# Kernel optimization log

Hardware: AMD Instinct MI355X
Metric: run time of the kernel (lower is better)

## Reference

```python
import jax, jax.numpy as jnp
import numpy as np

BATCH = 128
VOCAB = 128000


def setup_inputs() -> dict:
    key = jax.random.key(0)
    k1, k2, k3, k4 = jax.random.split(key, 4)
    logits = jax.random.normal(k1, (BATCH, VOCAB), dtype=jnp.float32)
    # per-row top-k in [1, VOCAB] (k == VOCAB means "no top-k filtering")
    k = jax.random.randint(k2, (BATCH,), 1, VOCAB + 1, dtype=jnp.int64)
    # per-row top-p in (0, 1)
    p = jax.random.uniform(k3, (BATCH,), dtype=jnp.float32, minval=0.05, maxval=0.99)
    # exponential noise for Gumbel-like weighted sampling (vLLM random_sample)
    exp_noise = jax.random.exponential(k4, (BATCH, VOCAB), dtype=jnp.float32)
    return {"logits": logits, "k": k, "p": p, "exp_noise": exp_noise}


def _apply_top_k_top_p(logits, k, p):
    vocab = logits.shape[1]
    probs = jax.nn.softmax(logits, axis=-1)           # [B, V]
    probs_sort = jnp.sort(probs, axis=-1)             # ascending, [B, V]

    # --- top-k: find cutoff = k-th largest prob (ties included) ---
    top_k_count = (vocab - k.astype(jnp.int32))[:, None]          # [B, 1]
    top_k_cutoff = jnp.take_along_axis(probs_sort, top_k_count, axis=-1)  # [B, 1]
    no_top_k_mask = (k.astype(jnp.int32) == vocab)[:, None]
    top_k_cutoff = jnp.where(no_top_k_mask, -jnp.inf, top_k_cutoff)
    logits = jnp.where(probs < top_k_cutoff, -jnp.inf, logits)

    # --- top-p: cutoff = smallest prob kept so that kept mass >= p ---
    cumprob = jnp.cumsum(probs_sort, axis=-1)                      # [B, V]
    top_p_mask = cumprob <= (1.0 - p[:, None])
    top_p_mask = top_p_mask.at[:, -1].set(False)  # keep at least one token
    top_p_count = jnp.sum(top_p_mask, axis=-1, keepdims=True)      # [B, 1]
    top_p_cutoff = jnp.take_along_axis(probs_sort, top_p_count, axis=-1)
    logits = jnp.where(probs < top_p_cutoff, -jnp.inf, logits)
    return logits


def reference(logits, k, p, exp_noise):
    filtered = _apply_top_k_top_p(logits, k, p)
    probs = jax.nn.softmax(filtered.astype(jnp.float32), axis=-1)  # [B, V]
    # vLLM random_sample: probs / Exp(1) noise, argmax == categorical draw
    samples = jnp.argmax(probs / exp_noise, axis=-1)               # [B]
    return samples
```

## Files before the change

### kernel.cpp

```cpp
#include <hip/hip_runtime.h>
#include <math.h>
#include <limits.h>

#define V 128000
#define R 128
#define NB 4096
#define NT 1024
#define SLICES 4
#define SLICE (V / SLICES)
#define S4 (SLICE / 4)
#define CAP 1024
#define BPT (NB / NT)

typedef unsigned long long u64;

struct Rec {
    u64   Tu;
    u64   psPu;
    float rowmax;
    float Lcut;
    int   binK;
    int   rankK;
    int   binP;
    int   binP2;
    unsigned pcP;
    unsigned minP2;
    int   nK;
    int   nP;
};

__device__ __forceinline__ int binof(float x) {
    int b = (int)floorf((x + 8.0f) * 256.0f);
    b = b < 0 ? 0 : b;
    b = b > NB - 1 ? NB - 1 : b;
    return b;
}

__device__ __forceinline__ u64 expq(float x) {
    float xc = fminf(x, 14.0f);
    return (u64)(expf(xc) * 16777216.0f);
}

__device__ __forceinline__ unsigned fmono(float x) {
    unsigned b = __float_as_uint(x);
    return b ^ ((b >> 31) ? 0xFFFFFFFFu : 0x80000000u);
}
__device__ __forceinline__ float fmono_inv(unsigned m) {
    unsigned b = (m & 0x80000000u) ? (m ^ 0x80000000u) : ~m;
    return __uint_as_float(b);
}

__device__ __forceinline__ bool better(float v1, int i1, float v2, int i2) {
    bool n1 = (v1 != v1), n2 = (v2 != v2);
    if (n1 != n2) return n1;
    if (n1) return i1 < i2;
    if (v1 != v2) return v1 > v2;
    return i1 < i2;
}

__global__ __launch_bounds__(NT) void k1_hist(
    const float* __restrict__ logits,
    unsigned* __restrict__ histCnt, u64* __restrict__ histSum,
    float* __restrict__ sliceMax)
{
    const int row = blockIdx.x / SLICES;
    const int sl  = blockIdx.x % SLICES;
    const int tid = threadIdx.x;
    const float4* l4 = reinterpret_cast<const float4*>(logits + (size_t)row * V) + (size_t)sl * S4;

    __shared__ unsigned hc[NB];
    __shared__ u64      hs[NB];
    __shared__ float    redf[NT];

    for (int i = tid; i < NB; i += NT) { hc[i] = 0u; hs[i] = 0ull; }
    __syncthreads();

    float lmax = -INFINITY;
    for (int i = tid; i < S4; i += NT) {
        float4 q = l4[i];
        float xs[4] = {q.x, q.y, q.z, q.w};
        #pragma unroll
        for (int c = 0; c < 4; ++c) {
            float x = xs[c];
            lmax = fmaxf(lmax, x);
            int b = binof(x);
            atomicAdd(&hc[b], 1u);
            atomicAdd(&hs[b], expq(x));
        }
    }
    redf[tid] = lmax;
    __syncthreads();
    for (int s = NT / 2; s > 0; s >>= 1) {
        if (tid < s) redf[tid] = fmaxf(redf[tid], redf[tid + s]);
        __syncthreads();
    }

    unsigned* gc = histCnt + ((size_t)sl * R + row) * NB;
    u64*      gs = histSum + ((size_t)sl * R + row) * NB;
    for (int i = tid; i < NB; i += NT) { gc[i] = hc[i]; gs[i] = hs[i]; }
    if (tid == 0) sliceMax[row * SLICES + sl] = redf[0];
}

__global__ __launch_bounds__(NT) void k2a_scan(
    const unsigned* __restrict__ histCnt, const u64* __restrict__ histSum,
    const float* __restrict__ sliceMax,
    const int* __restrict__ kk, const float* __restrict__ pp,
    Rec* __restrict__ rec)
{
    const int row = blockIdx.x;
    const int tid = threadIdx.x;

    __shared__ unsigned hcnt[NB];
    __shared__ u64      hsum[NB];
    __shared__ unsigned chCnt[NT];
    __shared__ u64      chSum[NT];
    __shared__ u64 s_psPu;
    __shared__ int s_binK, s_rankK, s_binP, s_binP2;
    __shared__ unsigned s_pcP;

    if (tid == 0) {
        s_binK = -1; s_rankK = 0; s_binP = -1; s_binP2 = NB;
        s_pcP = 0u; s_psPu = 0ull;
    }

    for (int i = tid; i < NB; i += NT) {
        unsigned c = 0; u64 s = 0ull;
        #pragma unroll
        for (int sl = 0; sl < SLICES; ++sl) {
            c += histCnt[((size_t)sl * R + row) * NB + i];
            s += histSum[((size_t)sl * R + row) * NB + i];
        }
        hcnt[i] = c; hsum[i] = s;
    }
    __syncthreads();

    const int kv = kk[row];
    const float pv = pp[row];

    unsigned cc = 0; u64 cs = 0ull;
    #pragma unroll
    for (int j = 0; j < BPT; ++j) { cc += hcnt[tid * BPT + j]; cs += hsum[tid * BPT + j]; }
    chCnt[tid] = cc; chSum[tid] = cs;
    __syncthreads();
    for (int off = 1; off < NT; off <<= 1) {
        unsigned uc = chCnt[tid]; u64 uf = chSum[tid];
        unsigned ac = (tid >= off) ? chCnt[tid - off] : 0u;
        u64      af = (tid >= off) ? chSum[tid - off] : 0ull;
        __syncthreads();
        chCnt[tid] = uc + ac; chSum[tid] = uf + af;
        __syncthreads();
    }
    const u64 Zu = chSum[NT - 1];
    const float omp = 1.0f - pv;
    const u64 Tu = (u64)((double)omp * (double)Zu);

    {
        unsigned pc = (tid > 0) ? chCnt[tid - 1] : 0u;
        u64 ps = (tid > 0) ? chSum[tid - 1] : 0ull;
        const unsigned rk = (unsigned)(V - kv);
        #pragma unroll
        for (int j = 0; j < BPT; ++j) {
            int bin = tid * BPT + j;
            unsigned c = hcnt[bin]; u64 s = hsum[bin];
            if (kv < V && c > 0u && rk >= pc && rk < pc + c) {
                s_binK = bin; s_rankK = (int)(rk - pc);
            }
            if (c > 0u && ps <= Tu && ps + s > Tu) {
                if (atomicCAS(&s_binP, -1, bin) == -1) { s_pcP = pc; s_psPu = ps; }
            }
            pc += c; ps += s;
        }
    }
    __syncthreads();
    if (tid == 0 && s_binP < 0) {
        unsigned pc = 0u; u64 ps = 0ull;
        int lastb = -1; unsigned lastpc = 0u; u64 lastps = 0ull;
        for (int b = 0; b < NB; ++b) {
            unsigned c = hcnt[b]; u64 s = hsum[b];
            if (c > 0u) {
                if (ps <= Tu && ps + s > Tu) { s_binP = b; s_pcP = pc; s_psPu = ps; break; }
                lastb = b; lastpc = pc; lastps = ps;
            }
            pc += c; ps += s;
        }
        if (s_binP < 0) { s_binP = lastb; s_pcP = lastpc; s_psPu = lastps; }
    }
    __syncthreads();
    {
        const int bp = s_binP;
        #pragma unroll
        for (int j = 0; j < BPT; ++j) {
            int bin = tid * BPT + j;
            if (bin > bp && hcnt[bin] > 0u) atomicMin(&s_binP2, bin);
        }
    }
    __syncthreads();

    if (tid == 0) {
        float rm = sliceMax[row * SLICES + 0];
        #pragma unroll
        for (int sl = 1; sl < SLICES; ++sl) rm = fmaxf(rm, sliceMax[row * SLICES + sl]);
        Rec rc;
        rc.Tu = Tu; rc.psPu = s_psPu;
        rc.rowmax = rm; rc.Lcut = -INFINITY;
        rc.binK = s_binK; rc.rankK = s_rankK; rc.binP = s_binP; rc.binP2 = s_binP2;
        rc.pcP = s_pcP; rc.minP2 = 0xFFFFFFFFu; rc.nK = 0; rc.nP = 0;
        rec[row] = rc;
    }
}

__global__ __launch_bounds__(NT) void k2b_collect(
    const float* __restrict__ logits, Rec* __restrict__ rec,
    float* __restrict__ candK, float* __restrict__ candP)
{
    const int row = blockIdx.x / SLICES;
    const int sl  = blockIdx.x % SLICES;
    const int tid = threadIdx.x;
    const float4* l4 = reinterpret_cast<const float4*>(logits + (size_t)row * V) + (size_t)sl * S4;

    const int bK = rec[row].binK, bP = rec[row].binP, bP2 = rec[row].binP2;
    float* cK = candK + (size_t)row * CAP;
    float* cP = candP + (size_t)row * CAP;

    for (int i = tid; i < S4; i += NT) {
        float4 q = l4[i];
        float xs[4] = {q.x, q.y, q.z, q.w};
        #pragma unroll
        for (int c = 0; c < 4; ++c) {
            float x = xs[c];
            int b = binof(x);
            if (b == bK) { int pos = atomicAdd(&rec[row].nK, 1); if (pos < CAP) cK[pos] = x; }
            if (b == bP) { int pos = atomicAdd(&rec[row].nP, 1); if (pos < CAP) cP[pos] = x; }
            if (b == bP2) atomicMin(&rec[row].minP2, fmono(x));
        }
    }
}

__global__ __launch_bounds__(NT) void k2c_cutoff(
    const int* __restrict__ kk, Rec* __restrict__ rec,
    const float* __restrict__ candK, const float* __restrict__ candP)
{
    const int row = blockIdx.x;
    const int tid = threadIdx.x;

    __shared__ float lcK[CAP];
    __shared__ float lcP[CAP];
    __shared__ float sorted[CAP];
    __shared__ float s_cutK;

    if (tid == 0) s_cutK = -INFINITY;
    const int kv = kk[row];
    const Rec rc = rec[row];
    const int nK = min(rc.nK, CAP), nP = min(rc.nP, CAP);

    if (tid < nK) lcK[tid] = candK[(size_t)row * CAP + tid];
    if (tid < nP) lcP[tid] = candP[(size_t)row * CAP + tid];
    __syncthreads();

    if (kv < V && tid < nK) {
        float v = lcK[tid];
        int r = 0;
        for (int j = 0; j < nK; ++j) {
            float u = lcK[j];
            r += (int)((u < v) | ((u == v) & (j < tid)));
        }
        if (r == rc.rankK) s_cutK = v;
    }
    if (tid < nP) {
        float v = lcP[tid];
        int r = 0;
        for (int j = 0; j < nP; ++j) {
            float u = lcP[j];
            r += (int)((u < v) | ((u == v) & (j < tid)));
        }
        sorted[r] = v;
    }
    __syncthreads();

    if (tid == 0) {
        float cutP;
        if (nP <= 0) {
            cutP = -INFINITY;
        } else {
            u64 cum = rc.psPu; int cin = 0;
            while (cin < nP) {
                u64 nc = cum + expq(sorted[cin]);
                if (nc <= rc.Tu) { cum = nc; ++cin; } else break;
            }
            long cglob = (long)rc.pcP + cin;
            if (cglob > (long)(V - 1)) cglob = V - 1;
            int local = (int)(cglob - (long)rc.pcP);
            cutP = (local < nP) ? sorted[local] : fmono_inv(rc.minP2);
        }
        float cutK = (kv < V) ? s_cutK : -INFINITY;
        rec[row].Lcut = fmaxf(cutK, cutP);
    }
}

__global__ __launch_bounds__(NT) void k3_argmax(
    const float* __restrict__ logits, const float* __restrict__ noise,
    const Rec* __restrict__ rec, float* __restrict__ partV, int* __restrict__ partI)
{
    const int row = blockIdx.x / SLICES;
    const int sl  = blockIdx.x % SLICES;
    const int tid = threadIdx.x;
    const float4* l4 = reinterpret_cast<const float4*>(logits + (size_t)row * V) + (size_t)sl * S4;
    const float4* n4 = reinterpret_cast<const float4*>(noise  + (size_t)row * V) + (size_t)sl * S4;
    const int base = sl * SLICE;

    __shared__ float redf[NT];
    __shared__ int   redi[NT];

    const float Lcut = rec[row].Lcut, rmax = rec[row].rowmax;
    float bv = -INFINITY; int bi = INT_MAX;
    for (int i = tid; i < S4; i += NT) {
        float4 lq = l4[i];
        float4 nq = n4[i];
        float ls[4] = {lq.x, lq.y, lq.z, lq.w};
        float ns[4] = {nq.x, nq.y, nq.z, nq.w};
        #pragma unroll
        for (int c = 0; c < 4; ++c) {
            int idx = base + 4 * i + c;
            float prob = (ls[c] >= Lcut) ? expf(ls[c] - rmax) : 0.0f;
            float r = prob / ns[c];
            if (better(r, idx, bv, bi)) { bv = r; bi = idx; }
        }
    }
    redf[tid] = bv; redi[tid] = bi;
    __syncthreads();
    for (int s = NT / 2; s > 0; s >>= 1) {
        if (tid < s) {
            if (better(redf[tid + s], redi[tid + s], redf[tid], redi[tid])) {
                redf[tid] = redf[tid + s]; redi[tid] = redi[tid + s];
            }
        }
        __syncthreads();
    }
    if (tid == 0) { partV[row * SLICES + sl] = redf[0]; partI[row * SLICES + sl] = redi[0]; }
}

__global__ __launch_bounds__(R) void k4_final(
    const float* __restrict__ partV, const int* __restrict__ partI, int* __restrict__ out)
{
    const int row = threadIdx.x;
    float bv = partV[row * SLICES + 0]; int bi = partI[row * SLICES + 0];
    #pragma unroll
    for (int sl = 1; sl < SLICES; ++sl) {
        float v = partV[row * SLICES + sl]; int i = partI[row * SLICES + sl];
        if (better(v, i, bv, bi)) { bv = v; bi = i; }
    }
    out[row] = bi;
}

__global__ __launch_bounds__(NT) void topk_topp_sample_mono(
    const float* __restrict__ logits, const int* __restrict__ kk,
    const float* __restrict__ pp, const float* __restrict__ noise,
    int* __restrict__ out)
{
    const int row = blockIdx.x;
    const int tid = threadIdx.x;
    const float4* l4 = reinterpret_cast<const float4*>(logits + (size_t)row * V);
    const float4* n4 = reinterpret_cast<const float4*>(noise  + (size_t)row * V);

    __shared__ unsigned hcnt[NB];
    __shared__ u64      hsum[NB];
    __shared__ unsigned chCnt[NT];
    __shared__ u64      chSum[NT];
    __shared__ float    redf[NT];
    __shared__ int      redi[NT];
    __shared__ float    candK[CAP];
    __shared__ float    candP[CAP];
    __shared__ float s_rowmax, s_cutK, s_Lcut;
    __shared__ u64 s_psPu;
    __shared__ int s_binK, s_rankK, s_binP, s_binP2, s_nK, s_nP;
    __shared__ unsigned s_pcP, s_minP2;

    const int kv = kk[row];
    const float pv = pp[row];

    for (int i = tid; i < NB; i += NT) { hcnt[i] = 0u; hsum[i] = 0ull; }
    if (tid == 0) {
        s_binK = -1; s_rankK = 0; s_binP = -1; s_binP2 = NB;
        s_nK = 0; s_nP = 0; s_minP2 = 0xFFFFFFFFu; s_cutK = -INFINITY;
        s_pcP = 0u; s_psPu = 0ull;
    }
    __syncthreads();

    float lmax = -INFINITY;
    for (int i = tid; i < V / 4; i += NT) {
        float4 q = l4[i];
        float xs[4] = {q.x, q.y, q.z, q.w};
        #pragma unroll
        for (int c = 0; c < 4; ++c) {
            float x = xs[c];
            lmax = fmaxf(lmax, x);
            int b = binof(x);
            atomicAdd(&hcnt[b], 1u);
            atomicAdd(&hsum[b], expq(x));
        }
    }
    redf[tid] = lmax;
    __syncthreads();
    for (int s = NT / 2; s > 0; s >>= 1) {
        if (tid < s) redf[tid] = fmaxf(redf[tid], redf[tid + s]);
        __syncthreads();
    }
    if (tid == 0) s_rowmax = redf[0];

    unsigned cc = 0; u64 cs = 0ull;
    #pragma unroll
    for (int j = 0; j < BPT; ++j) { cc += hcnt[tid * BPT + j]; cs += hsum[tid * BPT + j]; }
    chCnt[tid] = cc; chSum[tid] = cs;
    __syncthreads();
    for (int off = 1; off < NT; off <<= 1) {
        unsigned uc = chCnt[tid]; u64 uf = chSum[tid];
        unsigned ac = (tid >= off) ? chCnt[tid - off] : 0u;
        u64      af = (tid >= off) ? chSum[tid - off] : 0ull;
        __syncthreads();
        chCnt[tid] = uc + ac; chSum[tid] = uf + af;
        __syncthreads();
    }
    const u64 Zu = chSum[NT - 1];
    const float omp = 1.0f - pv;
    const u64 Tu = (u64)((double)omp * (double)Zu);

    {
        unsigned pc = (tid > 0) ? chCnt[tid - 1] : 0u;
        u64 ps = (tid > 0) ? chSum[tid - 1] : 0ull;
        const unsigned rk = (unsigned)(V - kv);
        #pragma unroll
        for (int j = 0; j < BPT; ++j) {
            int bin = tid * BPT + j;
            unsigned c = hcnt[bin]; u64 s = hsum[bin];
            if (kv < V && c > 0u && rk >= pc && rk < pc + c) {
                s_binK = bin; s_rankK = (int)(rk - pc);
            }
            if (c > 0u && ps <= Tu && ps + s > Tu) {
                if (atomicCAS(&s_binP, -1, bin) == -1) { s_pcP = pc; s_psPu = ps; }
            }
            pc += c; ps += s;
        }
    }
    __syncthreads();
    if (tid == 0 && s_binP < 0) {
        unsigned pc = 0u; u64 ps = 0ull;
        int lastb = -1; unsigned lastpc = 0u; u64 lastps = 0ull;
        for (int b = 0; b < NB; ++b) {
            unsigned c = hcnt[b]; u64 s = hsum[b];
            if (c > 0u) {
                if (ps <= Tu && ps + s > Tu) { s_binP = b; s_pcP = pc; s_psPu = ps; break; }
                lastb = b; lastpc = pc; lastps = ps;
            }
            pc += c; ps += s;
        }
        if (s_binP < 0) { s_binP = lastb; s_pcP = lastpc; s_psPu = lastps; }
    }
    __syncthreads();
    {
        const int bp = s_binP;
        #pragma unroll
        for (int j = 0; j < BPT; ++j) {
            int bin = tid * BPT + j;
            if (bin > bp && hcnt[bin] > 0u) atomicMin(&s_binP2, bin);
        }
    }
    __syncthreads();

    {
        const int bK = s_binK, bP = s_binP, bP2 = s_binP2;
        for (int i = tid; i < V / 4; i += NT) {
            float4 q = l4[i];
            float xs[4] = {q.x, q.y, q.z, q.w};
            #pragma unroll
            for (int c = 0; c < 4; ++c) {
                float x = xs[c];
                int b = binof(x);
                if (b == bK) { int pos = atomicAdd(&s_nK, 1); if (pos < CAP) candK[pos] = x; }
                if (b == bP) { int pos = atomicAdd(&s_nP, 1); if (pos < CAP) candP[pos] = x; }
                if (b == bP2) atomicMin(&s_minP2, fmono(x));
            }
        }
    }
    __syncthreads();

    const int nK = min(s_nK, CAP), nP = min(s_nP, CAP);
    if (kv < V && tid < nK) {
        float v = candK[tid];
        int r = 0;
        for (int j = 0; j < nK; ++j) {
            float u = candK[j];
            r += (int)((u < v) | ((u == v) & (j < tid)));
        }
        if (r == s_rankK) s_cutK = v;
    }
    if (tid < nP) {
        float v = candP[tid];
        int r = 0;
        for (int j = 0; j < nP; ++j) {
            float u = candP[j];
            r += (int)((u < v) | ((u == v) & (j < tid)));
        }
        redf[r] = v;
    }
    __syncthreads();
    if (tid == 0) {
        float cutP;
        if (nP <= 0) {
            cutP = -INFINITY;
        } else {
            u64 cum = s_psPu; int cin = 0;
            while (cin < nP) {
                u64 nc = cum + expq(redf[cin]);
                if (nc <= Tu) { cum = nc; ++cin; } else break;
            }
            long cglob = (long)s_pcP + cin;
            if (cglob > (long)(V - 1)) cglob = V - 1;
            int local = (int)(cglob - (long)s_pcP);
            cutP = (local < nP) ? redf[local] : fmono_inv(s_minP2);
        }
        float cutK = (kv < V) ? s_cutK : -INFINITY;
        s_Lcut = fmaxf(cutK, cutP);
    }
    __syncthreads();

    const float Lcut = s_Lcut, rmax = s_rowmax;
    float bv = -INFINITY; int bi = INT_MAX;
    for (int i = tid; i < V / 4; i += NT) {
        float4 lq = l4[i];
        float4 nq = n4[i];
        float ls[4] = {lq.x, lq.y, lq.z, lq.w};
        float ns[4] = {nq.x, nq.y, nq.z, nq.w};
        #pragma unroll
        for (int c = 0; c < 4; ++c) {
            int idx = 4 * i + c;
            float prob = (ls[c] >= Lcut) ? expf(ls[c] - rmax) : 0.0f;
            float r = prob / ns[c];
            if (better(r, idx, bv, bi)) { bv = r; bi = idx; }
        }
    }
    redf[tid] = bv; redi[tid] = bi;
    __syncthreads();
    for (int s = NT / 2; s > 0; s >>= 1) {
        if (tid < s) {
            if (better(redf[tid + s], redi[tid + s], redf[tid], redi[tid])) {
                redf[tid] = redf[tid + s]; redi[tid] = redi[tid + s];
            }
        }
        __syncthreads();
    }
    if (tid == 0) out[row] = redi[0];
}

static inline size_t alignup(size_t x) { return (x + 255) & ~(size_t)255; }

extern "C" void kernel_launch(void* const* d_in, const int* in_sizes, int n_in,
                              void* d_out, int out_size, void* d_ws, size_t ws_size,
                              hipStream_t stream) {
    const float* logits = (const float*)d_in[0];
    const int*   kk     = (const int*)d_in[1];
    const float* pp     = (const float*)d_in[2];
    const float* noise  = (const float*)d_in[3];
    int* out = (int*)d_out;
    char* ws = (char*)d_ws;

    size_t o = 0;
    size_t histCntOff = o; o = alignup(o + (size_t)SLICES * R * NB * 4);
    size_t histSumOff = o; o = alignup(o + (size_t)SLICES * R * NB * 8);
    size_t sliceMaxOff = o; o = alignup(o + (size_t)R * SLICES * 4);
    size_t recOff = o; o = alignup(o + (size_t)R * sizeof(Rec));
    size_t candKOff = o; o = alignup(o + (size_t)R * CAP * 4);
    size_t candPOff = o; o = alignup(o + (size_t)R * CAP * 4);
    size_t partVOff = o; o = alignup(o + (size_t)R * SLICES * 4);
    size_t partIOff = o; o = alignup(o + (size_t)R * SLICES * 4);

    if (ws_size >= o) {
        unsigned* histCnt = (unsigned*)(ws + histCntOff);
        u64*      histSum = (u64*)(ws + histSumOff);
        float*    sliceMax = (float*)(ws + sliceMaxOff);
        Rec*      rec = (Rec*)(ws + recOff);
        float*    candK = (float*)(ws + candKOff);
        float*    candP = (float*)(ws + candPOff);
        float*    partV = (float*)(ws + partVOff);
        int*      partI = (int*)(ws + partIOff);
        k1_hist<<<R * SLICES, NT, 0, stream>>>(logits, histCnt, histSum, sliceMax);
        k2a_scan<<<R, NT, 0, stream>>>(histCnt, histSum, sliceMax, kk, pp, rec);
        k2b_collect<<<R * SLICES, NT, 0, stream>>>(logits, rec, candK, candP);
        k2c_cutoff<<<R, NT, 0, stream>>>(kk, rec, candK, candP);
        k3_argmax<<<R * SLICES, NT, 0, stream>>>(logits, noise, rec, partV, partI);
        k4_final<<<1, R, 0, stream>>>(partV, partI, out);
        return;
    }
    topk_topp_sample_mono<<<R, NT, 0, stream>>>(logits, kk, pp, noise, out);
}
```

Baseline: 112.6 us.

## Fuse scan, collect and cutoff kernels; fold final argmax into last-arriving block

Merges the histogram scan, candidate collection and cutoff computation into one per-row kernel that keeps candidates and counters in shared memory instead of global atomics and workspace. The final per-row reduction kernel is removed: the last slice block of each row, detected via an atomic counter, combines the partial argmaxes. This cuts two kernel launches and the global round trips for the row record and candidate buffers. In exchange, collection now scans each row's logits with only 128 blocks instead of 512, which lowers parallelism on that pass.

```diff
diff --git a/kernel.cpp b/kernel.cpp
--- a/kernel.cpp
+++ b/kernel.cpp
@@ -14,19 +14,9 @@
 
 typedef unsigned long long u64;
 
-struct Rec {
-    u64   Tu;
-    u64   psPu;
+struct Cut {
+    float Lcut;
     float rowmax;
-    float Lcut;
-    int   binK;
-    int   rankK;
-    int   binP;
-    int   binP2;
-    unsigned pcP;
-    unsigned minP2;
-    int   nK;
-    int   nP;
 };
 
 __device__ __forceinline__ int binof(float x) {
@@ -101,11 +91,11 @@
     if (tid == 0) sliceMax[row * SLICES + sl] = redf[0];
 }
 
-__global__ __launch_bounds__(NT) void k2a_scan(
+__global__ __launch_bounds__(NT) void k2_cutoff(
     const unsigned* __restrict__ histCnt, const u64* __restrict__ histSum,
-    const float* __restrict__ sliceMax,
-    const int* __restrict__ kk, const float* __restrict__ pp,
-    Rec* __restrict__ rec)
+    const float* __restrict__ sliceMax, const int* __restrict__ kk,
+    const float* __restrict__ pp, const float* __restrict__ logits,
+    Cut* __restrict__ cut, unsigned* __restrict__ counters)
 {
     const int row = blockIdx.x;
     const int tid = threadIdx.x;
@@ -114,13 +104,18 @@
     __shared__ u64      hsum[NB];
     __shared__ unsigned chCnt[NT];
     __shared__ u64      chSum[NT];
+    __shared__ float    candK[CAP];
+    __shared__ float    candP[CAP];
+    __shared__ float    sorted[CAP];
     __shared__ u64 s_psPu;
-    __shared__ int s_binK, s_rankK, s_binP, s_binP2;
-    __shared__ unsigned s_pcP;
+    __shared__ float s_cutK;
+    __shared__ int s_binK, s_rankK, s_binP, s_binP2, s_nK, s_nP;
+    __shared__ unsigned s_pcP, s_minP2;
 
     if (tid == 0) {
         s_binK = -1; s_rankK = 0; s_binP = -1; s_binP2 = NB;
         s_pcP = 0u; s_psPu = 0ull;
+        s_nK = 0; s_nP = 0; s_minP2 = 0xFFFFFFFFu; s_cutK = -INFINITY;
     }
 
     for (int i = tid; i < NB; i += NT) {
@@ -196,81 +191,39 @@
     }
     __syncthreads();
 
-    if (tid == 0) {
-        float rm = sliceMax[row * SLICES + 0];
-        #pragma unroll
-        for (int sl = 1; sl < SLICES; ++sl) rm = fmaxf(rm, sliceMax[row * SLICES + sl]);
-        Rec rc;
-        rc.Tu = Tu; rc.psPu = s_psPu;
-        rc.rowmax = rm; rc.Lcut = -INFINITY;
-        rc.binK = s_binK; rc.rankK = s_rankK; rc.binP = s_binP; rc.binP2 = s_binP2;
-        rc.pcP = s_pcP; rc.minP2 = 0xFFFFFFFFu; rc.nK = 0; rc.nP = 0;
-        rec[row] = rc;
-    }
-}
-
-__global__ __launch_bounds__(NT) void k2b_collect(
-    const float* __restrict__ logits, Rec* __restrict__ rec,
-    float* __restrict__ candK, float* __restrict__ candP)
-{
-    const int row = blockIdx.x / SLICES;
-    const int sl  = blockIdx.x % SLICES;
-    const int tid = threadIdx.x;
-    const float4* l4 = reinterpret_cast<const float4*>(logits + (size_t)row * V) + (size_t)sl * S4;
-
-    const int bK = rec[row].binK, bP = rec[row].binP, bP2 = rec[row].binP2;
-    float* cK = candK + (size_t)row * CAP;
-    float* cP = candP + (size_t)row * CAP;
-
-    for (int i = tid; i < S4; i += NT) {
-        float4 q = l4[i];
-        float xs[4] = {q.x, q.y, q.z, q.w};
-        #pragma unroll
-        for (int c = 0; c < 4; ++c) {
-            float x = xs[c];
-            int b = binof(x);
-            if (b == bK) { int pos = atomicAdd(&rec[row].nK, 1); if (pos < CAP) cK[pos] = x; }
-            if (b == bP) { int pos = atomicAdd(&rec[row].nP, 1); if (pos < CAP) cP[pos] = x; }
-            if (b == bP2) atomicMin(&rec[row].minP2, fmono(x));
-        }
-    }
-}
-
-__global__ __launch_bounds__(NT) void k2c_cutoff(
-    const int* __restrict__ kk, Rec* __restrict__ rec,
-    const float* __restrict__ candK, const float* __restrict__ candP)
-{
-    const int row = blockIdx.x;
-    const int tid = threadIdx.x;
-
-    __shared__ float lcK[CAP];
-    __shared__ float lcP[CAP];
-    __shared__ float sorted[CAP];
-    __shared__ float s_cutK;
-
-    if (tid == 0) s_cutK = -INFINITY;
-    const int kv = kk[row];
-    const Rec rc = rec[row];
-    const int nK = min(rc.nK, CAP), nP = min(rc.nP, CAP);
-
-    if (tid < nK) lcK[tid] = candK[(size_t)row * CAP + tid];
-    if (tid < nP) lcP[tid] = candP[(size_t)row * CAP + tid];
-    __syncthreads();
-
+    {
+        const int bK = s_binK, bP = s_binP, bP2 = s_binP2;
+        const float4* l4 = reinterpret_cast<const float4*>(logits + (size_t)row * V);
+        for (int i = tid; i < V / 4; i += NT) {
+            float4 q = l4[i];
+            float xs[4] = {q.x, q.y, q.z, q.w};
+            #pragma unroll
+            for (int c = 0; c < 4; ++c) {
+                float x = xs[c];
+                int b = binof(x);
+                if (b == bK) { int pos = atomicAdd(&s_nK, 1); if (pos < CAP) candK[pos] = x; }
+                if (b == bP) { int pos = atomicAdd(&s_nP, 1); if (pos < CAP) candP[pos] = x; }
+                if (b == bP2) atomicMin(&s_minP2, fmono(x));
+            }
+        }
+    }
+    __syncthreads();
+
+    const int nK = min(s_nK, CAP), nP = min(s_nP, CAP);
     if (kv < V && tid < nK) {
-        float v = lcK[tid];
+        float v = candK[tid];
         int r = 0;
         for (int j = 0; j < nK; ++j) {
-            float u = lcK[j];
+            float u = candK[j];
             r += (int)((u < v) | ((u == v) & (j < tid)));
         }
-        if (r == rc.rankK) s_cutK = v;
+        if (r == s_rankK) s_cutK = v;
     }
     if (tid < nP) {
-        float v = lcP[tid];
+        float v = candP[tid];
         int r = 0;
         for (int j = 0; j < nP; ++j) {
-            float u = lcP[j];
+            float u = candP[j];
             r += (int)((u < v) | ((u == v) & (j < tid)));
         }
         sorted[r] = v;
@@ -282,24 +235,30 @@
         if (nP <= 0) {
             cutP = -INFINITY;
         } else {
-            u64 cum = rc.psPu; int cin = 0;
+            u64 cum = s_psPu; int cin = 0;
             while (cin < nP) {
                 u64 nc = cum + expq(sorted[cin]);
-                if (nc <= rc.Tu) { cum = nc; ++cin; } else break;
-            }
-            long cglob = (long)rc.pcP + cin;
+                if (nc <= Tu) { cum = nc; ++cin; } else break;
+            }
+            long cglob = (long)s_pcP + cin;
             if (cglob > (long)(V - 1)) cglob = V - 1;
-            int local = (int)(cglob - (long)rc.pcP);
-            cutP = (local < nP) ? sorted[local] : fmono_inv(rc.minP2);
+            int local = (int)(cglob - (long)s_pcP);
+            cutP = (local < nP) ? sorted[local] : fmono_inv(s_minP2);
         }
         float cutK = (kv < V) ? s_cutK : -INFINITY;
-        rec[row].Lcut = fmaxf(cutK, cutP);
+        float rm = sliceMax[row * SLICES + 0];
+        #pragma unroll
+        for (int sl = 1; sl < SLICES; ++sl) rm = fmaxf(rm, sliceMax[row * SLICES + sl]);
+        Cut c; c.Lcut = fmaxf(cutK, cutP); c.rowmax = rm;
+        cut[row] = c;
+        counters[row] = 0u;
     }
 }
 
 __global__ __launch_bounds__(NT) void k3_argmax(
     const float* __restrict__ logits, const float* __restrict__ noise,
-    const Rec* __restrict__ rec, float* __restrict__ partV, int* __restrict__ partI)
+    const Cut* __restrict__ cut, float* __restrict__ partV, int* __restrict__ partI,
+    unsigned* __restrict__ counters, int* __restrict__ out)
 {
     const int row = blockIdx.x / SLICES;
     const int sl  = blockIdx.x % SLICES;
@@ -311,7 +270,7 @@
     __shared__ float redf[NT];
     __shared__ int   redi[NT];
 
-    const float Lcut = rec[row].Lcut, rmax = rec[row].rowmax;
+    const float Lcut = cut[row].Lcut, rmax = cut[row].rowmax;
     float bv = -INFINITY; int bi = INT_MAX;
     for (int i = tid; i < S4; i += NT) {
         float4 lq = l4[i];
@@ -336,20 +295,24 @@
         }
         __syncthreads();
     }
-    if (tid == 0) { partV[row * SLICES + sl] = redf[0]; partI[row * SLICES + sl] = redi[0]; }
-}
-
-__global__ __launch_bounds__(R) void k4_final(
-    const float* __restrict__ partV, const int* __restrict__ partI, int* __restrict__ out)
-{
-    const int row = threadIdx.x;
-    float bv = partV[row * SLICES + 0]; int bi = partI[row * SLICES + 0];
-    #pragma unroll
-    for (int sl = 1; sl < SLICES; ++sl) {
-        float v = partV[row * SLICES + sl]; int i = partI[row * SLICES + sl];
-        if (better(v, i, bv, bi)) { bv = v; bi = i; }
-    }
-    out[row] = bi;
+    if (tid == 0) {
+        partV[row * SLICES + sl] = redf[0];
+        partI[row * SLICES + sl] = redi[0];
+        __threadfence();
+        unsigned old = atomicAdd(&counters[row], 1u);
+        if (old == SLICES - 1) {
+            __threadfence();
+            volatile const float* pv = partV + row * SLICES;
+            volatile const int*   pi = partI + row * SLICES;
+            float fv = pv[0]; int fi = pi[0];
+            #pragma unroll
+            for (int s2 = 1; s2 < SLICES; ++s2) {
+                float v = pv[s2]; int i2 = pi[s2];
+                if (better(v, i2, fv, fi)) { fv = v; fi = i2; }
+            }
+            out[row] = fi;
+        }
+    }
 }
 
 __global__ __launch_bounds__(NT) void topk_topp_sample_mono(
@@ -567,27 +530,22 @@
     size_t histCntOff = o; o = alignup(o + (size_t)SLICES * R * NB * 4);
     size_t histSumOff = o; o = alignup(o + (size_t)SLICES * R * NB * 8);
     size_t sliceMaxOff = o; o = alignup(o + (size_t)R * SLICES * 4);
-    size_t recOff = o; o = alignup(o + (size_t)R * sizeof(Rec));
-    size_t candKOff = o; o = alignup(o + (size_t)R * CAP * 4);
-    size_t candPOff = o; o = alignup(o + (size_t)R * CAP * 4);
+    size_t cutOff = o; o = alignup(o + (size_t)R * sizeof(Cut));
     size_t partVOff = o; o = alignup(o + (size_t)R * SLICES * 4);
     size_t partIOff = o; o = alignup(o + (size_t)R * SLICES * 4);
+    size_t cntrOff = o; o = alignup(o + (size_t)R * 4);
 
     if (ws_size >= o) {
         unsigned* histCnt = (unsigned*)(ws + histCntOff);
         u64*      histSum = (u64*)(ws + histSumOff);
         float*    sliceMax = (float*)(ws + sliceMaxOff);
-        Rec*      rec = (Rec*)(ws + recOff);
-        float*    candK = (float*)(ws + candKOff);
-        float*    candP = (float*)(ws + candPOff);
+        Cut*      cut = (Cut*)(ws + cutOff);
         float*    partV = (float*)(ws + partVOff);
         int*      partI = (int*)(ws + partIOff);
+        unsigned* counters = (unsigned*)(ws + cntrOff);
         k1_hist<<<R * SLICES, NT, 0, stream>>>(logits, histCnt, histSum, sliceMax);
-        k2a_scan<<<R, NT, 0, stream>>>(histCnt, histSum, sliceMax, kk, pp, rec);
-        k2b_collect<<<R * SLICES, NT, 0, stream>>>(logits, rec, candK, candP);
-        k2c_cutoff<<<R, NT, 0, stream>>>(kk, rec, candK, candP);
-        k3_argmax<<<R * SLICES, NT, 0, stream>>>(logits, noise, rec, partV, partI);
-        k4_final<<<1, R, 0, stream>>>(partV, partI, out);
+        k2_cutoff<<<R, NT, 0, stream>>>(histCnt, histSum, sliceMax, kk, pp, logits, cut, counters);
+        k3_argmax<<<R * SLICES, NT, 0, stream>>>(logits, noise, cut, partV, partI, counters, out);
         return;
     }
     topk_topp_sample_mono<<<R, NT, 0, stream>>>(logits, kk, pp, noise, out);
```

New measurement: 127.3 us. 1.13x slower.

## Fuse cutoff computation and final reduction into argmax kernel

Applied to the files above, without the earlier changes.

The separate cutoff kernel is folded into the argmax kernel, so each slice block recomputes the per-row cutoff from the candidate lists in shared memory. The final cross-slice reduction kernel is replaced by a last-block-done pattern that uses an atomic counter and thread fences. This removes two kernel launches and their inter-kernel gaps. In exchange the O(CAP^2) candidate ranking is now done four times per row, once per slice block.

```diff
diff --git a/kernel.cpp b/kernel.cpp
--- a/kernel.cpp
+++ b/kernel.cpp
@@ -18,7 +18,6 @@
     u64   Tu;
     u64   psPu;
     float rowmax;
-    float Lcut;
     int   binK;
     int   rankK;
     int   binP;
@@ -105,7 +104,7 @@
     const unsigned* __restrict__ histCnt, const u64* __restrict__ histSum,
     const float* __restrict__ sliceMax,
     const int* __restrict__ kk, const float* __restrict__ pp,
-    Rec* __restrict__ rec)
+    Rec* __restrict__ rec, unsigned* __restrict__ counters)
 {
     const int row = blockIdx.x;
     const int tid = threadIdx.x;
@@ -201,11 +200,11 @@
         #pragma unroll
         for (int sl = 1; sl < SLICES; ++sl) rm = fmaxf(rm, sliceMax[row * SLICES + sl]);
         Rec rc;
-        rc.Tu = Tu; rc.psPu = s_psPu;
-        rc.rowmax = rm; rc.Lcut = -INFINITY;
+        rc.Tu = Tu; rc.psPu = s_psPu; rc.rowmax = rm;
         rc.binK = s_binK; rc.rankK = s_rankK; rc.binP = s_binP; rc.binP2 = s_binP2;
         rc.pcP = s_pcP; rc.minP2 = 0xFFFFFFFFu; rc.nK = 0; rc.nP = 0;
         rec[row] = rc;
+        counters[row] = 0u;
     }
 }
 
@@ -236,17 +235,26 @@
     }
 }
 
-__global__ __launch_bounds__(NT) void k2c_cutoff(
-    const int* __restrict__ kk, Rec* __restrict__ rec,
-    const float* __restrict__ candK, const float* __restrict__ candP)
+__global__ __launch_bounds__(NT) void k3_argmax(
+    const float* __restrict__ logits, const float* __restrict__ noise,
+    const int* __restrict__ kk, const Rec* __restrict__ rec,
+    const float* __restrict__ candK, const float* __restrict__ candP,
+    float* __restrict__ partV, int* __restrict__ partI,
+    unsigned* __restrict__ counters, int* __restrict__ out)
 {
-    const int row = blockIdx.x;
+    const int row = blockIdx.x / SLICES;
+    const int sl  = blockIdx.x % SLICES;
     const int tid = threadIdx.x;
+    const float4* l4 = reinterpret_cast<const float4*>(logits + (size_t)row * V) + (size_t)sl * S4;
+    const float4* n4 = reinterpret_cast<const float4*>(noise  + (size_t)row * V) + (size_t)sl * S4;
+    const int base = sl * SLICE;
 
     __shared__ float lcK[CAP];
     __shared__ float lcP[CAP];
     __shared__ float sorted[CAP];
-    __shared__ float s_cutK;
+    __shared__ float redf[NT];
+    __shared__ int   redi[NT];
+    __shared__ float s_cutK, s_Lcut;
 
     if (tid == 0) s_cutK = -INFINITY;
     const int kv = kk[row];
@@ -276,7 +284,6 @@
         sorted[r] = v;
     }
     __syncthreads();
-
     if (tid == 0) {
         float cutP;
         if (nP <= 0) {
@@ -293,25 +300,11 @@
             cutP = (local < nP) ? sorted[local] : fmono_inv(rc.minP2);
         }
         float cutK = (kv < V) ? s_cutK : -INFINITY;
-        rec[row].Lcut = fmaxf(cutK, cutP);
-    }
-}
-
-__global__ __launch_bounds__(NT) void k3_argmax(
-    const float* __restrict__ logits, const float* __restrict__ noise,
-    const Rec* __restrict__ rec, float* __restrict__ partV, int* __restrict__ partI)
-{
-    const int row = blockIdx.x / SLICES;
-    const int sl  = blockIdx.x % SLICES;
-    const int tid = threadIdx.x;
-    const float4* l4 = reinterpret_cast<const float4*>(logits + (size_t)row * V) + (size_t)sl * S4;
-    const float4* n4 = reinterpret_cast<const float4*>(noise  + (size_t)row * V) + (size_t)sl * S4;
-    const int base = sl * SLICE;
-
-    __shared__ float redf[NT];
-    __shared__ int   redi[NT];
-
-    const float Lcut = rec[row].Lcut, rmax = rec[row].rowmax;
+        s_Lcut = fmaxf(cutK, cutP);
+    }
+    __syncthreads();
+
+    const float Lcut = s_Lcut, rmax = rc.rowmax;
     float bv = -INFINITY; int bi = INT_MAX;
     for (int i = tid; i < S4; i += NT) {
         float4 lq = l4[i];
@@ -336,20 +329,24 @@
         }
         __syncthreads();
     }
-    if (tid == 0) { partV[row * SLICES + sl] = redf[0]; partI[row * SLICES + sl] = redi[0]; }
-}
-
-__global__ __launch_bounds__(R) void k4_final(
-    const float* __restrict__ partV, const int* __restrict__ partI, int* __restrict__ out)
-{
-    const int row = threadIdx.x;
-    float bv = partV[row * SLICES + 0]; int bi = partI[row * SLICES + 0];
-    #pragma unroll
-    for (int sl = 1; sl < SLICES; ++sl) {
-        float v = partV[row * SLICES + sl]; int i = partI[row * SLICES + sl];
-        if (better(v, i, bv, bi)) { bv = v; bi = i; }
-    }
-    out[row] = bi;
+    if (tid == 0) {
+        partV[row * SLICES + sl] = redf[0];
+        partI[row * SLICES + sl] = redi[0];
+        __threadfence();
+        unsigned old = atomicAdd(&counters[row], 1u);
+        if (old == SLICES - 1) {
+            __threadfence();
+            volatile const float* pv = partV + row * SLICES;
+            volatile const int*   pi = partI + row * SLICES;
+            float fv = pv[0]; int fi = pi[0];
+            #pragma unroll
+            for (int s2 = 1; s2 < SLICES; ++s2) {
+                float v = pv[s2]; int i2 = pi[s2];
+                if (better(v, i2, fv, fi)) { fv = v; fi = i2; }
+            }
+            out[row] = fi;
+        }
+    }
 }
 
 __global__ __launch_bounds__(NT) void topk_topp_sample_mono(
@@ -572,6 +569,7 @@
     size_t candPOff = o; o = alignup(o + (size_t)R * CAP * 4);
     size_t partVOff = o; o = alignup(o + (size_t)R * SLICES * 4);
     size_t partIOff = o; o = alignup(o + (size_t)R * SLICES * 4);
+    size_t cntrOff = o; o = alignup(o + (size_t)R * 4);
 
     if (ws_size >= o) {
         unsigned* histCnt = (unsigned*)(ws + histCntOff);
@@ -582,12 +580,12 @@
         float*    candP = (float*)(ws + candPOff);
         float*    partV = (float*)(ws + partVOff);
         int*      partI = (int*)(ws + partIOff);
+        unsigned* counters = (unsigned*)(ws + cntrOff);
         k1_hist<<<R * SLICES, NT, 0, stream>>>(logits, histCnt, histSum, sliceMax);
-        k2a_scan<<<R, NT, 0, stream>>>(histCnt, histSum, sliceMax, kk, pp, rec);
+        k2a_scan<<<R, NT, 0, stream>>>(histCnt, histSum, sliceMax, kk, pp, rec, counters);
         k2b_collect<<<R * SLICES, NT, 0, stream>>>(logits, rec, candK, candP);
-        k2c_cutoff<<<R, NT, 0, stream>>>(kk, rec, candK, candP);
-        k3_argmax<<<R * SLICES, NT, 0, stream>>>(logits, noise, rec, partV, partI);
-        k4_final<<<1, R, 0, stream>>>(partV, partI, out);
+        k3_argmax<<<R * SLICES, NT, 0, stream>>>(logits, noise, kk, rec, candK, candP,
+                                                 partV, partI, counters, out);
         return;
     }
     topk_topp_sample_mono<<<R, NT, 0, stream>>>(logits, kk, pp, noise, out);
```

After: 140.8 us. 25.0% more time.
